# Performance work log

Measured on AMD Instinct MI355X. Metric: run time of the kernel, lower is better.

Reference implementation:

```python
import jax, jax.numpy as jnp
import numpy as np

B = 8388608
F = 5


def setup_inputs() -> dict:
    key = jax.random.key(0)
    k1, k2 = jax.random.split(key)
    outputs = jax.random.normal(k1, (B, F), dtype=jnp.float32)
    targets = jax.random.uniform(k2, (B, F), dtype=jnp.float32)
    return {"outputs": outputs, "targets": targets}


def reference(outputs, targets):
    # columns 1..4 are circular (angles normalized to [0,1)); column 0 is linear
    F_ = outputs.shape[1]
    circ = (jnp.arange(F_) >= 1) & (jnp.arange(F_) <= 4)  # [F]
    out = jnp.where(circ, jnp.mod(outputs, 1.0), outputs)
    # wrap target toward output when the circular distance exceeds 0.5
    shift = jnp.where(jnp.abs(out - targets) > 0.5,
                      jnp.where(targets < out, 1.0, -1.0),
                      0.0)
    tgt = jnp.where(circ, targets + shift, targets)
    return jnp.mean((out - tgt) ** 2)
```

## Files before the change

kernel.cpp:

```cpp
#include <hip/hip_runtime.h>


constexpr unsigned int BDIM = 8388608u;
constexpr unsigned int FDIM = 5u;
constexpr unsigned int NTOT = BDIM * FDIM;
constexpr unsigned int NCHUNK = NTOT / 4u;
constexpr int NBLOCKS = 2048;
constexpr int NTHREADS = 256;

__global__ __launch_bounds__(NTHREADS) void moonloss_partial(
    const float* __restrict__ outp,
    const float* __restrict__ tgtp,
    float* __restrict__ partial) {
  unsigned int tid = blockIdx.x * blockDim.x + threadIdx.x;
  unsigned int stride = gridDim.x * blockDim.x;

  float acc = 0.0f;
  for (unsigned int c = tid; c < NCHUNK; c += stride) {
    float4 o4 = reinterpret_cast<const float4*>(outp)[c];
    float4 t4 = reinterpret_cast<const float4*>(tgtp)[c];
    float o[4] = {o4.x, o4.y, o4.z, o4.w};
    float t[4] = {t4.x, t4.y, t4.z, t4.w};
    unsigned int base = c * 4u;
#pragma unroll
    for (int j = 0; j < 4; ++j) {
      unsigned int col = (base + (unsigned int)j) % FDIM;
      float oo = o[j];
      float tt = t[j];
      bool circ = (col != 0u);
      if (circ) oo = oo - floorf(oo);
      float d = oo - tt;
      float shift = (fabsf(d) > 0.5f) ? ((tt < oo) ? 1.0f : -1.0f) : 0.0f;
      float tw = circ ? (tt + shift) : tt;
      float diff = oo - tw;
      acc = fmaf(diff, diff, acc);
    }
  }

#pragma unroll
  for (int off = 32; off > 0; off >>= 1) acc += __shfl_down(acc, off, 64);

  __shared__ float sacc[NTHREADS / 64];
  int wid = threadIdx.x >> 6;
  if ((threadIdx.x & 63) == 0) sacc[wid] = acc;
  __syncthreads();
  if (threadIdx.x == 0) {
    float s = 0.0f;
#pragma unroll
    for (int w = 0; w < NTHREADS / 64; ++w) s += sacc[w];
    partial[blockIdx.x] = s;
  }
}

__global__ __launch_bounds__(256) void moonloss_final(
    const float* __restrict__ partial, int n, float* __restrict__ out) {
  double acc = 0.0;
  for (int i = threadIdx.x; i < n; i += blockDim.x) acc += (double)partial[i];
  __shared__ double s[256];
  s[threadIdx.x] = acc;
  __syncthreads();
  for (int off = 128; off > 0; off >>= 1) {
    if (threadIdx.x < off) s[threadIdx.x] += s[threadIdx.x + off];
    __syncthreads();
  }
  if (threadIdx.x == 0) out[0] = (float)(s[0] / (double)NTOT);
}

extern "C" void kernel_launch(void* const* d_in, const int* in_sizes, int n_in,
                              void* d_out, int out_size, void* d_ws, size_t ws_size,
                              hipStream_t stream) {
  const float* outputs = (const float*)d_in[0];
  const float* targets = (const float*)d_in[1];
  float* out = (float*)d_out;
  float* partial = (float*)d_ws;

  moonloss_partial<<<NBLOCKS, NTHREADS, 0, stream>>>(outputs, targets, partial);
  moonloss_final<<<1, 256, 0, stream>>>(partial, NBLOCKS, out);
}
```

Measured before the change: 336.5 us.

## Software-pipeline grid-stride loads with double-buffered register batches

Replaces the grid-stride loop with a fully unrolled sequence of five batches, each holding four float4 pairs. Two register buffers alternate, so the next batch is loading while the current one is being computed. The goal is more memory-level parallelism per thread to hide HBM latency. In exchange, the trip count is fixed at compile time by a static_assert, and register pressure rises under launch_bounds occupancy 4.

```diff
diff --git a/kernel.cpp b/kernel.cpp
--- a/kernel.cpp
+++ b/kernel.cpp
@@ -1,41 +1,80 @@
 #include <hip/hip_runtime.h>
 
 
-constexpr unsigned int BDIM = 8388608u;
-constexpr unsigned int FDIM = 5u;
-constexpr unsigned int NTOT = BDIM * FDIM;
-constexpr unsigned int NCHUNK = NTOT / 4u;
+constexpr unsigned FDIM = 5u;
+constexpr unsigned NTOT = 41943040u;
+constexpr unsigned NCHUNK = NTOT / 4u;
 constexpr int NBLOCKS = 2048;
 constexpr int NTHREADS = 256;
+constexpr unsigned STRIDE = (unsigned)NBLOCKS * NTHREADS;
+constexpr int ITERS = (int)(NCHUNK / STRIDE);
+constexpr int BATCH = 4;
 
-__global__ __launch_bounds__(NTHREADS) void moonloss_partial(
+__device__ __forceinline__ float chunk_loss(float4 o4, float4 t4,
+                                            unsigned base, float acc) {
+  float o[4] = {o4.x, o4.y, o4.z, o4.w};
+  float t[4] = {t4.x, t4.y, t4.z, t4.w};
+#pragma unroll
+  for (int j = 0; j < 4; ++j) {
+    unsigned col = (base + (unsigned)j) % FDIM;
+    float oo = o[j];
+    float tt = t[j];
+    bool circ = (col != 0u);
+    if (circ) oo = oo - floorf(oo);
+    float d = oo - tt;
+    float shift = (fabsf(d) > 0.5f) ? ((tt < oo) ? 1.0f : -1.0f) : 0.0f;
+    float tw = circ ? (tt + shift) : tt;
+    float diff = oo - tw;
+    acc = fmaf(diff, diff, acc);
+  }
+  return acc;
+}
+
+__device__ __forceinline__ void load_batch(const float4* __restrict__ op,
+                                           const float4* __restrict__ tp,
+                                           unsigned tid, int b,
+                                           float4 (&o)[BATCH], float4 (&t)[BATCH]) {
+#pragma unroll
+  for (int j = 0; j < BATCH; ++j) {
+    unsigned c = tid + (unsigned)(b * BATCH + j) * STRIDE;
+    o[j] = op[c];
+    t[j] = tp[c];
+  }
+}
+
+__device__ __forceinline__ float comp_batch(unsigned tid, int b,
+                                            const float4 (&o)[BATCH],
+                                            const float4 (&t)[BATCH], float acc) {
+#pragma unroll
+  for (int j = 0; j < BATCH; ++j) {
+    unsigned c = tid + (unsigned)(b * BATCH + j) * STRIDE;
+    acc = chunk_loss(o[j], t[j], c * 4u, acc);
+  }
+  return acc;
+}
+
+__global__ __launch_bounds__(NTHREADS, 4) void moonloss_partial(
     const float* __restrict__ outp,
     const float* __restrict__ tgtp,
     float* __restrict__ partial) {
-  unsigned int tid = blockIdx.x * blockDim.x + threadIdx.x;
-  unsigned int stride = gridDim.x * blockDim.x;
+  unsigned tid = blockIdx.x * (unsigned)NTHREADS + threadIdx.x;
+  const float4* op = reinterpret_cast<const float4*>(outp);
+  const float4* tp = reinterpret_cast<const float4*>(tgtp);
 
   float acc = 0.0f;
-  for (unsigned int c = tid; c < NCHUNK; c += stride) {
-    float4 o4 = reinterpret_cast<const float4*>(outp)[c];
-    float4 t4 = reinterpret_cast<const float4*>(tgtp)[c];
-    float o[4] = {o4.x, o4.y, o4.z, o4.w};
-    float t[4] = {t4.x, t4.y, t4.z, t4.w};
-    unsigned int base = c * 4u;
-#pragma unroll
-    for (int j = 0; j < 4; ++j) {
-      unsigned int col = (base + (unsigned int)j) % FDIM;
-      float oo = o[j];
-      float tt = t[j];
-      bool circ = (col != 0u);
-      if (circ) oo = oo - floorf(oo);
-      float d = oo - tt;
-      float shift = (fabsf(d) > 0.5f) ? ((tt < oo) ? 1.0f : -1.0f) : 0.0f;
-      float tw = circ ? (tt + shift) : tt;
-      float diff = oo - tw;
-      acc = fmaf(diff, diff, acc);
-    }
-  }
+  float4 oA[BATCH], tA[BATCH], oB[BATCH], tB[BATCH];
+
+  static_assert(ITERS == 20 && BATCH == 4, "sequence below assumes 5 batches");
+  load_batch(op, tp, tid, 0, oA, tA);
+  load_batch(op, tp, tid, 1, oB, tB);
+  acc = comp_batch(tid, 0, oA, tA, acc);
+  load_batch(op, tp, tid, 2, oA, tA);
+  acc = comp_batch(tid, 1, oB, tB, acc);
+  load_batch(op, tp, tid, 3, oB, tB);
+  acc = comp_batch(tid, 2, oA, tA, acc);
+  load_batch(op, tp, tid, 4, oA, tA);
+  acc = comp_batch(tid, 3, oB, tB, acc);
+  acc = comp_batch(tid, 4, oA, tA, acc);
 
 #pragma unroll
   for (int off = 32; off > 0; off >>= 1) acc += __shfl_down(acc, off, 64);
```

New measurement: 338.8 us. About the same (+0.7%).

## Stream inputs through LDS with async global_load_lds multi-stage pipeline

Applied to the files above, without the earlier changes.

Replaces direct float4 global loads with asynchronous global-to-LDS copies (global_load_lds), keeping four tiles in flight per thread and waiting on explicit vmcnt counts. The grid-stride loop is fully unrolled into a fixed 20-step sequence. The goal is deeper memory-level parallelism on a bandwidth-bound reduction. It hardcodes the iteration count, relies on hand-placed waitcnt and schedule barriers, and spends LDS that may reduce occupancy.

```diff
diff --git a/kernel.cpp b/kernel.cpp
--- a/kernel.cpp
+++ b/kernel.cpp
@@ -1,41 +1,82 @@
 #include <hip/hip_runtime.h>
 
 
-constexpr unsigned int BDIM = 8388608u;
-constexpr unsigned int FDIM = 5u;
-constexpr unsigned int NTOT = BDIM * FDIM;
-constexpr unsigned int NCHUNK = NTOT / 4u;
+constexpr unsigned FDIM = 5u;
+constexpr unsigned NTOT = 41943040u;
+constexpr unsigned NCHUNK = NTOT / 4u;
 constexpr int NBLOCKS = 2048;
 constexpr int NTHREADS = 256;
+constexpr unsigned STRIDE = (unsigned)NBLOCKS * NTHREADS;
+constexpr int ITERS = (int)(NCHUNK / STRIDE);
+constexpr int DEPTH = 4;
+
+#define VMWAIT_(n) do { asm volatile("s_waitcnt vmcnt(" #n ")" ::: "memory"); \
+                        __builtin_amdgcn_sched_barrier(0); } while (0)
+#define VMWAIT(n) VMWAIT_(n)
+#define LGWAIT()  do { asm volatile("s_waitcnt lgkmcnt(0)" ::: "memory"); \
+                       __builtin_amdgcn_sched_barrier(0); } while (0)
+
+__device__ __forceinline__ void glds16(const float4* g, float4* l) {
+  __builtin_amdgcn_global_load_lds(
+      (const __attribute__((address_space(1))) void*)g,
+      (__attribute__((address_space(3))) void*)l, 16, 0, 0);
+}
+
+__device__ __forceinline__ float chunk_loss(float4 o4, float4 t4,
+                                            unsigned base, float acc) {
+  float o[4] = {o4.x, o4.y, o4.z, o4.w};
+  float t[4] = {t4.x, t4.y, t4.z, t4.w};
+#pragma unroll
+  for (int j = 0; j < 4; ++j) {
+    unsigned col = (base + (unsigned)j) % FDIM;
+    float oo = o[j];
+    float tt = t[j];
+    bool circ = (col != 0u);
+    if (circ) oo = oo - floorf(oo);
+    float d = oo - tt;
+    float shift = (fabsf(d) > 0.5f) ? ((tt < oo) ? 1.0f : -1.0f) : 0.0f;
+    float tw = circ ? (tt + shift) : tt;
+    float diff = oo - tw;
+    acc = fmaf(diff, diff, acc);
+  }
+  return acc;
+}
 
 __global__ __launch_bounds__(NTHREADS) void moonloss_partial(
     const float* __restrict__ outp,
     const float* __restrict__ tgtp,
     float* __restrict__ partial) {
-  unsigned int tid = blockIdx.x * blockDim.x + threadIdx.x;
-  unsigned int stride = gridDim.x * blockDim.x;
+  __shared__ float4 buf[DEPTH][2][NTHREADS];
+
+  const unsigned tid = threadIdx.x;
+  const unsigned wbase = tid & ~63u;
+  const unsigned gtid = blockIdx.x * (unsigned)NTHREADS + tid;
+  const float4* gos = reinterpret_cast<const float4*>(outp) + gtid;
+  const float4* gts = reinterpret_cast<const float4*>(tgtp) + gtid;
 
   float acc = 0.0f;
-  for (unsigned int c = tid; c < NCHUNK; c += stride) {
-    float4 o4 = reinterpret_cast<const float4*>(outp)[c];
-    float4 t4 = reinterpret_cast<const float4*>(tgtp)[c];
-    float o[4] = {o4.x, o4.y, o4.z, o4.w};
-    float t[4] = {t4.x, t4.y, t4.z, t4.w};
-    unsigned int base = c * 4u;
-#pragma unroll
-    for (int j = 0; j < 4; ++j) {
-      unsigned int col = (base + (unsigned int)j) % FDIM;
-      float oo = o[j];
-      float tt = t[j];
-      bool circ = (col != 0u);
-      if (circ) oo = oo - floorf(oo);
-      float d = oo - tt;
-      float shift = (fabsf(d) > 0.5f) ? ((tt < oo) ? 1.0f : -1.0f) : 0.0f;
-      float tw = circ ? (tt + shift) : tt;
-      float diff = oo - tw;
-      acc = fmaf(diff, diff, acc);
-    }
-  }
+
+#define ISSUE(k) do {                                                   \
+    glds16(gos + (unsigned)(k) * STRIDE, &buf[(k) % DEPTH][0][wbase]);  \
+    glds16(gts + (unsigned)(k) * STRIDE, &buf[(k) % DEPTH][1][wbase]);  \
+  } while (0)
+
+  ISSUE(0); ISSUE(1); ISSUE(2); ISSUE(3);
+
+#define STEPK(k, vm) do {                                               \
+    VMWAIT(vm);                               \
+    float4 o4 = buf[(k) % DEPTH][0][tid];                               \
+    float4 t4 = buf[(k) % DEPTH][1][tid];                               \
+    LGWAIT();                          \
+    if ((k) + DEPTH < ITERS) ISSUE((k) + DEPTH);                        \
+    acc = chunk_loss(o4, t4, (gtid + (unsigned)(k) * STRIDE) * 4u, acc);\
+  } while (0)
+
+  STEPK(0, 6);  STEPK(1, 6);  STEPK(2, 6);  STEPK(3, 6);  STEPK(4, 6);
+  STEPK(5, 6);  STEPK(6, 6);  STEPK(7, 6);  STEPK(8, 6);  STEPK(9, 6);
+  STEPK(10, 6); STEPK(11, 6); STEPK(12, 6); STEPK(13, 6); STEPK(14, 6);
+  STEPK(15, 6); STEPK(16, 6); STEPK(17, 4); STEPK(18, 2); STEPK(19, 0);
+  static_assert(ITERS == 20 && DEPTH == 4, "step sequence assumes 20 tiles");
 
 #pragma unroll
   for (int off = 32; off > 0; off >>= 1) acc += __shfl_down(acc, off, 64);
```

New measurement: 333.8 us. No clear change (-0.8%).
